# Kernel optimization log

Measured on AMD Instinct MI355X. Metric: run time of the kernel, lower is better.

The kernel has to match this reference:

```python
import jax, jax.numpy as jnp
import numpy as np

N = 2048; E = 65536; T = 6; F_IN = 2
H_ENC = 256; LAT = 128; H_DEC = 256
PRED = 6
MIN_X, MAX_X = 0.0, 1.0
MIN_Y, MAX_Y = 0.0, 1.0
MIN_EW, MAX_EW = 0.0, 0.5
VISUAL_RANGE = 0.5


def setup_inputs() -> dict:
    key = jax.random.key(0)
    ks = jax.random.split(key, 17)
    p = lambda k, shape: jax.random.normal(k, shape, jnp.float32) * 0.05
    return {
        "x_seq": jax.random.uniform(ks[0], (T, N, F_IN), jnp.float32),
        "edge_index_seq": jax.random.randint(ks[1], (T, 2, E), 0, N),
        "edge_weight_seq": jax.random.uniform(ks[2], (T, E), jnp.float32, 1e-3, 1.0),
        "h_enc": jnp.zeros((N, H_ENC), jnp.float32),
        "h_dec": jnp.zeros((N, H_DEC), jnp.float32),
        "enc_Wx": p(ks[3], (3, 2, F_IN, H_ENC)),
        "enc_bx": p(ks[4], (3, H_ENC)),
        "enc_Wh": p(ks[5], (3, 2, H_ENC, H_ENC)),
        "enc_bh": p(ks[6], (3, H_ENC)),
        "enc_lin_W": p(ks[7], (H_ENC, LAT)),
        "enc_lin_b": p(ks[8], (LAT,)),
        "dec_Wx": p(ks[9], (3, 2, LAT, H_DEC)),
        "dec_bx": p(ks[10], (3, H_DEC)),
        "dec_Wh": p(ks[11], (3, 2, H_DEC, H_DEC)),
        "dec_bh": p(ks[12], (3, H_DEC)),
        "dec_lin_W": p(ks[13], (H_DEC, F_IN)),
        "dec_lin_b": p(ks[14], (F_IN,)),
    }


def _sparse_conv_fn(edge_index, edge_weight, n):
    # ChebConv K=2, sym normalization, lambda_max=2 => T1(L_hat) = -D^-1/2 A D^-1/2
    src, dst = edge_index[0], edge_index[1]
    deg = jax.ops.segment_sum(edge_weight, src, num_segments=n)
    dinv = jnp.where(deg > 0, jax.lax.rsqrt(jnp.where(deg > 0, deg, 1.0)), 0.0)
    norm = -dinv[src] * edge_weight * dinv[dst]  # [E]

    def conv(x, W, b):  # W: [2, in, out]
        tx1 = jax.ops.segment_sum(norm[:, None] * x[src], dst, num_segments=n)
        return x @ W[0] + tx1 @ W[1] + b
    return conv


def _dense_conv_fn(y_hat):
    # graph rebuilt from detached predicted coords (radius graph, dense masked form)
    c = jax.lax.stop_gradient(y_hat)
    px = c[:, 0] * (MAX_X - MIN_X) + MIN_X
    py = c[:, 1] * (MAX_Y - MIN_Y) + MIN_Y
    coords = jnp.stack((px, py), axis=1)  # [N, 2]
    d = jnp.linalg.norm(coords[:, None, :] - coords[None, :, :], axis=2)  # [N, N]
    mask = (d < VISUAL_RANGE) & (d > 0)
    w = jnp.where(mask, (d - MIN_EW) / (MAX_EW - MIN_EW), 0.0)
    deg = w.sum(axis=1)
    dinv = jnp.where(deg > 0, jax.lax.rsqrt(jnp.where(deg > 0, deg, 1.0)), 0.0)
    M = -(dinv[:, None] * w) * dinv[None, :]  # scaled-Laplacian off-diagonal

    def conv(x, W, b):
        return x @ W[0] + (M @ x) @ W[1] + b
    return conv


def _gru(conv, x, H, Wx, bx, Wh, bh):
    # GConvGRU gates: each gate = conv_x(X) + conv_h(H)
    z = jax.nn.sigmoid(conv(x, Wx[0], bx[0]) + conv(H, Wh[0], bh[0]))
    r = jax.nn.sigmoid(conv(x, Wx[1], bx[1]) + conv(H, Wh[1], bh[1]))
    h_tilde = jnp.tanh(conv(x, Wx[2], bx[2]) + conv(H * r, Wh[2], bh[2]))
    return z * H + (1.0 - z) * h_tilde


def reference(x_seq, edge_index_seq, edge_weight_seq, h_enc, h_dec,
              enc_Wx, enc_bx, enc_Wh, enc_bh, enc_lin_W, enc_lin_b,
              dec_Wx, dec_bx, dec_Wh, dec_bh, dec_lin_W, dec_lin_b):
    n = x_seq.shape[1]

    def step(conv, x, he, hd):
        he0 = _gru(conv, x, he, enc_Wx, enc_bx, enc_Wh, enc_bh)
        z = jax.nn.relu(he0) @ enc_lin_W + enc_lin_b
        hd0 = _gru(conv, z, hd, dec_Wx, dec_bx, dec_Wh, dec_bh)
        y_hat = jax.nn.relu(hd0) @ dec_lin_W + dec_lin_b
        return y_hat, he0, hd0

    # observed snapshots (sparse edge-list graphs)
    for t in range(x_seq.shape[0]):
        conv = _sparse_conv_fn(edge_index_seq[t], edge_weight_seq[t], n)
        y_hat, h_enc, h_dec = step(conv, x_seq[t], h_enc, h_dec)

    preds = [y_hat]
    for _ in range(PRED - 1):
        conv = _dense_conv_fn(y_hat)
        y_hat, h_enc, h_dec = step(conv, y_hat, h_enc, h_dec)
        preds.append(y_hat)
    return jnp.stack(preds)  # [PRED, N, 2]
```

## Files before the change

### kernel.cpp

```cpp
#include <hip/hip_runtime.h>
#include <math.h>

#define NN 2048
#define EE 65536
#define T_OBS 6
#define FIN 2
#define HE 256
#define LT 128
#define PREDN 6
#define DMM_NZ 8
#define ZR_NZ 4
#define GT_NZ 8
#define LIN_NZ 8

typedef __attribute__((ext_vector_type(8))) short short8v;
typedef __attribute__((ext_vector_type(4))) float float4v;

static __device__ __forceinline__ unsigned short f2bf(float f) {
    union { float f; unsigned u; } v; v.f = f;
    unsigned r = v.u + 0x7fff + ((v.u >> 16) & 1);
    return (unsigned short)(r >> 16);
}

static __device__ __forceinline__ void bfsplit(float f, unsigned short& h,
                                               unsigned short& l) {
    unsigned u = __float_as_uint(f);
    h = (unsigned short)(u >> 16);
    float hf = __uint_as_float(u & 0xffff0000u);
    l = (unsigned short)(__float_as_uint(f - hf) >> 16);
}

__global__ void k_degcnt(const int* __restrict__ src, const int* __restrict__ dst,
                         const float* __restrict__ ew,
                         float* __restrict__ deg, int* __restrict__ cnt) {
    int e = blockIdx.x * blockDim.x + threadIdx.x;
    if (e < EE) {
        atomicAdd(&deg[src[e]], ew[e]);
        atomicAdd(&cnt[dst[e]], 1);
    }
}

__global__ void k_scan(const int* __restrict__ cnt, const float* __restrict__ deg,
                       int* __restrict__ roff, int* __restrict__ cur,
                       float* __restrict__ dinv) {
    __shared__ int part[256];
    int t = threadIdx.x;
#pragma unroll
    for (int i = t; i < NN; i += 256) {
        float d = deg[i];
        dinv[i] = d > 0.f ? 1.f / sqrtf(d) : 0.f;
    }
    int loc[8];
    int s = 0;
#pragma unroll
    for (int i = 0; i < 8; i++) { loc[i] = cnt[t * 8 + i]; s += loc[i]; }
    part[t] = s;
    __syncthreads();
    for (int off = 1; off < 256; off <<= 1) {
        int v = (t >= off) ? part[t - off] : 0;
        __syncthreads();
        part[t] += v;
        __syncthreads();
    }
    int run = (t == 0) ? 0 : part[t - 1];
#pragma unroll
    for (int i = 0; i < 8; i++) {
        int idx = t * 8 + i;
        roff[idx] = run;
        cur[idx] = run;
        run += loc[i];
    }
    if (t == 255) roff[NN] = run;
}

__global__ void k_scatter2(const int* __restrict__ src, const int* __restrict__ dst,
                           const float* __restrict__ ew, const float* __restrict__ dinv,
                           int* __restrict__ cur,
                           int* __restrict__ csr_src, float* __restrict__ csr_nrm) {
    int e = blockIdx.x * blockDim.x + threadIdx.x;
    if (e < EE) {
        int s = src[e], d = dst[e];
        int p = atomicAdd(&cur[d], 1);
        csr_src[p] = s;
        csr_nrm[p] = -dinv[s] * ew[e] * dinv[d];
    }
}

template <int F>
__global__ void k_spmm_v(const int* __restrict__ roff, const int* __restrict__ csr_src,
                         const float* __restrict__ csr_nrm,
                         const float* __restrict__ X, float* __restrict__ out) {
    int w = threadIdx.x >> 6, lane = threadIdx.x & 63;
    int nid = (blockIdx.x << 2) + w;
    int c = lane << 2;
    int s0 = roff[nid], s1 = roff[nid + 1];
    float4 acc = make_float4(0.f, 0.f, 0.f, 0.f);
    int s = s0;
    for (; s + 8 <= s1; s += 8) {
        int is[8]; float ws[8];
#pragma unroll
        for (int j = 0; j < 8; j++) { is[j] = csr_src[s + j]; ws[j] = csr_nrm[s + j]; }
        if (c < F) {
            float4 xv[8];
#pragma unroll
            for (int j = 0; j < 8; j++) xv[j] = *(const float4*)&X[(size_t)is[j] * F + c];
#pragma unroll
            for (int j = 0; j < 8; j++) {
                acc.x = fmaf(ws[j], xv[j].x, acc.x);
                acc.y = fmaf(ws[j], xv[j].y, acc.y);
                acc.z = fmaf(ws[j], xv[j].z, acc.z);
                acc.w = fmaf(ws[j], xv[j].w, acc.w);
            }
        }
    }
    for (; s < s1; ++s) {
        int i0 = csr_src[s]; float w0 = csr_nrm[s];
        if (c < F) {
            float4 xv = *(const float4*)&X[(size_t)i0 * F + c];
            acc.x = fmaf(w0, xv.x, acc.x);
            acc.y = fmaf(w0, xv.y, acc.y);
            acc.z = fmaf(w0, xv.z, acc.z);
            acc.w = fmaf(w0, xv.w, acc.w);
        }
    }
    if (c < F) *(float4*)&out[(size_t)nid * F + c] = acc;
}

__global__ void k_spmm2(const int* __restrict__ roff, const int* __restrict__ csr_src,
                        const float* __restrict__ csr_nrm,
                        const float* __restrict__ X, float* __restrict__ out) {
    int nid = blockIdx.x * blockDim.x + threadIdx.x;
    if (nid < NN) {
        int s0 = roff[nid], s1 = roff[nid + 1];
        float a0 = 0.f, a1 = 0.f;
        for (int s = s0; s < s1; ++s) {
            int i = csr_src[s]; float w = csr_nrm[s];
            float2 xv = *(const float2*)&X[2 * i];
            a0 = fmaf(w, xv.x, a0);
            a1 = fmaf(w, xv.y, a1);
        }
        out[2 * nid] = a0;
        out[2 * nid + 1] = a1;
    }
}

__global__ void k_ddeg(const float* __restrict__ c, float* __restrict__ dinv) {
    int i = blockIdx.x;
    int t = threadIdx.x;
    float xi = c[2 * i], yi = c[2 * i + 1];
    float s = 0.f;
    for (int j = t; j < NN; j += 256) {
        float dx = xi - c[2 * j], dy = yi - c[2 * j + 1];
        float d = sqrtf(dx * dx + dy * dy);
        if (d > 0.f && d < 0.5f) s += 2.f * d;
    }
    __shared__ float red[256];
    red[t] = s;
    __syncthreads();
    for (int off = 128; off > 0; off >>= 1) {
        if (t < off) red[t] += red[t + off];
        __syncthreads();
    }
    if (t == 0) {
        float d = red[0];
        dinv[i] = d > 0.f ? 1.f / sqrtf(d) : 0.f;
    }
}

__global__ void k_dM(const float* __restrict__ c, const float* __restrict__ dinv,
                     float* __restrict__ M, unsigned short* __restrict__ Mb) {
    int idx = blockIdx.x * blockDim.x + threadIdx.x;
    int i = idx >> 11, j = idx & (NN - 1);
    float dx = c[2 * i] - c[2 * j], dy = c[2 * i + 1] - c[2 * j + 1];
    float d = sqrtf(dx * dx + dy * dy);
    float w = (d > 0.f && d < 0.5f) ? 2.f * d : 0.f;
    float v = -(dinv[i] * w) * dinv[j];
    M[idx] = v;
    Mb[idx] = f2bf(v);
}

template <int F>
__global__ __launch_bounds__(256) void k_dmm_mf(
    const unsigned short* __restrict__ Mb, const float* __restrict__ X,
    float* __restrict__ pbuf)
{
    __shared__ __align__(16) unsigned short Ms[64][72];
    __shared__ __align__(16) unsigned short Xs[64][72];
    const int tid = threadIdx.x;
    const int wid = tid >> 6, lane = tid & 63;
    const int m0 = blockIdx.x << 6, n0 = blockIdx.y << 6;
    const int kb0 = blockIdx.z << 8;
    const int lr = lane & 15;
    const int kg = lane >> 4;
    float4v acc[4];
#pragma unroll
    for (int t = 0; t < 4; t++) acc[t] = (float4v){0.f, 0.f, 0.f, 0.f};

    for (int kb = kb0; kb < kb0 + 256; kb += 64) {
#pragma unroll
        for (int it = 0; it < 2; it++) {
            int i = tid + it * 256;
            int r = i >> 3, c8 = (i & 7) << 3;
            *(short8v*)&Ms[r][c8] =
                *(const short8v*)&Mb[(size_t)(m0 + r) * NN + kb + c8];
        }
#pragma unroll
        for (int it = 0; it < 2; it++) {
            int i = tid + it * 256;
            int k2 = (i & 31) << 1;
            int n4 = (i >> 5) << 2;
            float4 va = *(const float4*)&X[(size_t)(kb + k2) * F + n0 + n4];
            float4 vb = *(const float4*)&X[(size_t)(kb + k2 + 1) * F + n0 + n4];
            unsigned pk;
            pk = (unsigned)f2bf(va.x) | ((unsigned)f2bf(vb.x) << 16);
            *(unsigned*)&Xs[n4 + 0][k2] = pk;
            pk = (unsigned)f2bf(va.y) | ((unsigned)f2bf(vb.y) << 16);
            *(unsigned*)&Xs[n4 + 1][k2] = pk;
            pk = (unsigned)f2bf(va.z) | ((unsigned)f2bf(vb.z) << 16);
            *(unsigned*)&Xs[n4 + 2][k2] = pk;
            pk = (unsigned)f2bf(va.w) | ((unsigned)f2bf(vb.w) << 16);
            *(unsigned*)&Xs[n4 + 3][k2] = pk;
        }
        __syncthreads();
#pragma unroll
        for (int kh = 0; kh < 2; kh++) {
            int kk = kh * 32 + kg * 8;
            short8v a = *(const short8v*)&Ms[(wid << 4) + lr][kk];
#pragma unroll
            for (int t = 0; t < 4; t++) {
                short8v b = *(const short8v*)&Xs[(t << 4) + lr][kk];
                acc[t] = __builtin_amdgcn_mfma_f32_16x16x32_bf16(a, b, acc[t], 0, 0, 0);
            }
        }
        __syncthreads();
    }
    float* p = pbuf + (size_t)blockIdx.z * NN * F;
#pragma unroll
    for (int t = 0; t < 4; t++)
#pragma unroll
        for (int j = 0; j < 4; j++)
            p[(size_t)(m0 + (wid << 4) + (kg << 2) + j) * F + n0 + (t << 4) + lr] =
                acc[t][j];
}

template <int F, int NZ>
__global__ void k_redks(const float* __restrict__ pbuf, float* __restrict__ out) {
    const int TOT = NN * F / 4;
    int i = blockIdx.x * blockDim.x + threadIdx.x;
    if (i < TOT) {
        const float4* p = (const float4*)pbuf;
        float4 s = p[i];
#pragma unroll
        for (int z = 1; z < NZ; z++) {
            float4 v = p[(size_t)z * TOT + i];
            s.x += v.x; s.y += v.y; s.z += v.z; s.w += v.w;
        }
        ((float4*)out)[i] = s;
    }
}

__global__ void k_dmv2(const float* __restrict__ M, const float* __restrict__ X,
                       float* __restrict__ out) {
    int i = blockIdx.x;
    int t = threadIdx.x;
    float a0 = 0.f, a1 = 0.f;
    for (int j = t; j < NN; j += 256) {
        float m = M[i * NN + j];
        a0 = fmaf(m, X[2 * j], a0);
        a1 = fmaf(m, X[2 * j + 1], a1);
    }
    __shared__ float r0[256], r1[256];
    r0[t] = a0;
    r1[t] = a1;
    __syncthreads();
    for (int off = 128; off > 0; off >>= 1) {
        if (t < off) { r0[t] += r0[t + off]; r1[t] += r1[t + off]; }
        __syncthreads();
    }
    if (t == 0) { out[2 * i] = r0[0]; out[2 * i + 1] = r1[0]; }
}

template <bool RELU>
__device__ __forceinline__ void mfma_seg(
    unsigned short (*Ah)[40], unsigned short (*Al)[40],
    unsigned short (*Bh)[40], unsigned short (*Bl)[40],
    const float* __restrict__ A, int lda,
    const float* __restrict__ B, int ldb, int K,
    int m0, int tid, int wid, int lr, int kg, float4v (&acc)[4])
{
    for (int k0 = 0; k0 < K; k0 += 32) {
        {
            int r = tid >> 2, k8 = (tid & 3) << 3;
            const float* ap = &A[(size_t)(m0 + r) * lda + k0 + k8];
            float4 va = *(const float4*)ap;
            float4 vb = *(const float4*)(ap + 4);
            float v[8] = {va.x, va.y, va.z, va.w, vb.x, vb.y, vb.z, vb.w};
            short8v hv, lv;
#pragma unroll
            for (int j = 0; j < 8; j++) {
                float f = RELU ? fmaxf(v[j], 0.f) : v[j];
                unsigned short h, l;
                bfsplit(f, h, l);
                hv[j] = (short)h; lv[j] = (short)l;
            }
            *(short8v*)&Ah[r][k8] = hv;
            *(short8v*)&Al[r][k8] = lv;
        }
        {
            int k2 = (tid & 15) << 1;
            int n4 = (tid >> 4) << 2;
            const float* bp = &B[(size_t)(k0 + k2) * ldb + n4];
            float4 va = *(const float4*)bp;
            float4 vb = *(const float4*)(bp + ldb);
            float v0[4] = {va.x, va.y, va.z, va.w};
            float v1[4] = {vb.x, vb.y, vb.z, vb.w};
#pragma unroll
            for (int j = 0; j < 4; j++) {
                unsigned short h0, l0, h1, l1;
                bfsplit(v0[j], h0, l0);
                bfsplit(v1[j], h1, l1);
                *(unsigned*)&Bh[n4 + j][k2] = (unsigned)h0 | ((unsigned)h1 << 16);
                *(unsigned*)&Bl[n4 + j][k2] = (unsigned)l0 | ((unsigned)l1 << 16);
            }
        }
        __syncthreads();
        short8v ah = *(short8v*)&Ah[(wid << 4) + lr][kg << 3];
        short8v al = *(short8v*)&Al[(wid << 4) + lr][kg << 3];
#pragma unroll
        for (int t = 0; t < 4; t++) {
            short8v bh = *(short8v*)&Bh[(t << 4) + lr][kg << 3];
            short8v bl = *(short8v*)&Bl[(t << 4) + lr][kg << 3];
            acc[t] = __builtin_amdgcn_mfma_f32_16x16x32_bf16(ah, bh, acc[t], 0, 0, 0);
            acc[t] = __builtin_amdgcn_mfma_f32_16x16x32_bf16(ah, bl, acc[t], 0, 0, 0);
            acc[t] = __builtin_amdgcn_mfma_f32_16x16x32_bf16(al, bh, acc[t], 0, 0, 0);
        }
        __syncthreads();
    }
}

__global__ __launch_bounds__(256) void k_zr_ks(
    const float* __restrict__ A0, int K01, const float* __restrict__ A1,
    const float* __restrict__ H, const float* __restrict__ A3,
    const float* __restrict__ Wx, const float* __restrict__ Wh,
    float* __restrict__ pbuf)
{
    __shared__ __align__(16) unsigned short Ah[64][40], Al[64][40],
                                            Bh[64][40], Bl[64][40];
    int tid = threadIdx.x;
    int wid = tid >> 6, lane = tid & 63, lr = lane & 15, kg = lane >> 4;
    int m0 = blockIdx.x << 6;
    int g = blockIdx.y >> 2;
    int n0 = (blockIdx.y & 3) << 6;
    float4v acc[4];
#pragma unroll
    for (int t = 0; t < 4; t++) acc[t] = (float4v){0.f, 0.f, 0.f, 0.f};
    const float* As[4] = {A0, A1, H, A3};
    const int ldas[4] = {K01, K01, HE, HE};
    const float* Bs[4] = {
        Wx + (size_t)(g * 2 + 0) * K01 * HE + n0,
        Wx + (size_t)(g * 2 + 1) * K01 * HE + n0,
        Wh + (size_t)(g * 2 + 0) * HE * HE + n0,
        Wh + (size_t)(g * 2 + 1) * HE * HE + n0};
    const int Ks[4] = {K01, K01, HE, HE};
    int chunk = (2 * K01 + 2 * HE) / ZR_NZ;
    int lo = blockIdx.z * chunk, hi = lo + chunk;
    int off = 0;
#pragma unroll
    for (int s = 0; s < 4; s++) {
        int a = lo - off; a = a < 0 ? 0 : a;
        int b = hi - off; b = b > Ks[s] ? Ks[s] : b;
        if (b > a)
            mfma_seg<false>(Ah, Al, Bh, Bl, As[s] + a, ldas[s],
                            Bs[s] + (size_t)a * HE, HE, b - a,
                            m0, tid, wid, lr, kg, acc);
        off += Ks[s];
    }
    float* p = pbuf + (size_t)blockIdx.z * NN * 512;
    int cbase = (g << 8) + n0;
#pragma unroll
    for (int t = 0; t < 4; t++)
#pragma unroll
        for (int j = 0; j < 4; j++)
            p[(size_t)(m0 + (wid << 4) + (kg << 2) + j) * 512 + cbase + (t << 4) + lr] =
                acc[t][j];
}

__global__ void k_zr_ep(const float* __restrict__ pbuf,
                        const float* __restrict__ bx, const float* __restrict__ bh,
                        const float* __restrict__ H,
                        const float* __restrict__ x2, const float* __restrict__ ax2,
                        const float* __restrict__ Wx,
                        float* __restrict__ gz, float* __restrict__ hr)
{
    int i = blockIdx.x * 256 + threadIdx.x;
    const float4* p = (const float4*)pbuf;
    const size_t S = (size_t)NN * 512 / 4;
    float4 a = p[i];
#pragma unroll
    for (int z = 1; z < ZR_NZ; z++) {
        float4 v = p[(size_t)z * S + i];
        a.x += v.x; a.y += v.y; a.z += v.z; a.w += v.w;
    }
    int row = i >> 7, c = (i & 127) << 2;
    int g = c >> 8, cc = c & 255;
    if (Wx) {
        float x0 = x2[2 * row], x1 = x2[2 * row + 1];
        float q0 = ax2[2 * row], q1 = ax2[2 * row + 1];
        const float* W0 = Wx + (size_t)(g * 2 + 0) * FIN * HE;
        const float* W1 = Wx + (size_t)(g * 2 + 1) * FIN * HE;
        float4 w00 = *(const float4*)&W0[cc];
        float4 w01 = *(const float4*)&W0[HE + cc];
        float4 w10 = *(const float4*)&W1[cc];
        float4 w11 = *(const float4*)&W1[HE + cc];
        a.x += x0 * w00.x + x1 * w01.x + q0 * w10.x + q1 * w11.x;
        a.y += x0 * w00.y + x1 * w01.y + q0 * w10.y + q1 * w11.y;
        a.z += x0 * w00.z + x1 * w01.z + q0 * w10.z + q1 * w11.z;
        a.w += x0 * w00.w + x1 * w01.w + q0 * w10.w + q1 * w11.w;
    }
    float4 b0 = *(const float4*)&bx[c];
    float4 b1 = *(const float4*)&bh[c];
    float4 s;
    s.x = 1.f / (1.f + expf(-(a.x + b0.x + b1.x)));
    s.y = 1.f / (1.f + expf(-(a.y + b0.y + b1.y)));
    s.z = 1.f / (1.f + expf(-(a.z + b0.z + b1.z)));
    s.w = 1.f / (1.f + expf(-(a.w + b0.w + b1.w)));
    if (c < HE) {
        *(float4*)&gz[(size_t)row * HE + c] = s;
    } else {
        float4 h = *(const float4*)&H[(size_t)row * HE + cc];
        s.x *= h.x; s.y *= h.y; s.z *= h.z; s.w *= h.w;
        *(float4*)&hr[(size_t)row * HE + cc] = s;
    }
}

__global__ __launch_bounds__(256) void k_gt_ks(
    const float* __restrict__ A0, int K01, const float* __restrict__ A1,
    const float* __restrict__ hr, const float* __restrict__ A3,
    const float* __restrict__ Wx2, const float* __restrict__ Wh2,
    float* __restrict__ pbuf)
{
    __shared__ __align__(16) unsigned short Ah[64][40], Al[64][40],
                                            Bh[64][40], Bl[64][40];
    int tid = threadIdx.x;
    int wid = tid >> 6, lane = tid & 63, lr = lane & 15, kg = lane >> 4;
    int m0 = blockIdx.x << 6;
    int n0 = blockIdx.y << 6;
    float4v acc[4];
#pragma unroll
    for (int t = 0; t < 4; t++) acc[t] = (float4v){0.f, 0.f, 0.f, 0.f};
    const float* As[4] = {A0, A1, hr, A3};
    const int ldas[4] = {K01, K01, HE, HE};
    const float* Bs[4] = {
        Wx2 + n0,
        Wx2 + (size_t)K01 * HE + n0,
        Wh2 + n0,
        Wh2 + (size_t)HE * HE + n0};
    const int Ks[4] = {K01, K01, HE, HE};
    int chunk = (2 * K01 + 2 * HE) / GT_NZ;
    int lo = blockIdx.z * chunk, hi = lo + chunk;
    int off = 0;
#pragma unroll
    for (int s = 0; s < 4; s++) {
        int a = lo - off; a = a < 0 ? 0 : a;
        int b = hi - off; b = b > Ks[s] ? Ks[s] : b;
        if (b > a)
            mfma_seg<false>(Ah, Al, Bh, Bl, As[s] + a, ldas[s],
                            Bs[s] + (size_t)a * HE, HE, b - a,
                            m0, tid, wid, lr, kg, acc);
        off += Ks[s];
    }
    float* p = pbuf + (size_t)blockIdx.z * NN * HE;
#pragma unroll
    for (int t = 0; t < 4; t++)
#pragma unroll
        for (int j = 0; j < 4; j++)
            p[(size_t)(m0 + (wid << 4) + (kg << 2) + j) * HE + n0 + (t << 4) + lr] =
                acc[t][j];
}

__global__ void k_gt_ep(const float* __restrict__ pbuf,
                        const float* __restrict__ bx2, const float* __restrict__ bh2,
                        const float* __restrict__ gz,
                        const float* __restrict__ x2, const float* __restrict__ ax2,
                        const float* __restrict__ Wx2,
                        float* __restrict__ H)
{
    int i = blockIdx.x * 256 + threadIdx.x;
    const float4* p = (const float4*)pbuf;
    const size_t S = (size_t)NN * HE / 4;
    float4 a = p[i];
#pragma unroll
    for (int z = 1; z < GT_NZ; z++) {
        float4 v = p[(size_t)z * S + i];
        a.x += v.x; a.y += v.y; a.z += v.z; a.w += v.w;
    }
    int row = i >> 6, c = (i & 63) << 2;
    if (Wx2) {
        float x0 = x2[2 * row], x1 = x2[2 * row + 1];
        float q0 = ax2[2 * row], q1 = ax2[2 * row + 1];
        float4 w00 = *(const float4*)&Wx2[c];
        float4 w01 = *(const float4*)&Wx2[HE + c];
        float4 w10 = *(const float4*)&Wx2[2 * HE + c];
        float4 w11 = *(const float4*)&Wx2[3 * HE + c];
        a.x += x0 * w00.x + x1 * w01.x + q0 * w10.x + q1 * w11.x;
        a.y += x0 * w00.y + x1 * w01.y + q0 * w10.y + q1 * w11.y;
        a.z += x0 * w00.z + x1 * w01.z + q0 * w10.z + q1 * w11.z;
        a.w += x0 * w00.w + x1 * w01.w + q0 * w10.w + q1 * w11.w;
    }
    float4 b0 = *(const float4*)&bx2[c];
    float4 b1 = *(const float4*)&bh2[c];
    size_t idx = (size_t)row * HE + c;
    float4 z = *(const float4*)&gz[idx];
    float4 h = *(const float4*)&H[idx];
    float4 o;
    o.x = z.x * h.x + (1.f - z.x) * tanhf(a.x + b0.x + b1.x);
    o.y = z.y * h.y + (1.f - z.y) * tanhf(a.y + b0.y + b1.y);
    o.z = z.z * h.z + (1.f - z.z) * tanhf(a.z + b0.z + b1.z);
    o.w = z.w * h.w + (1.f - z.w) * tanhf(a.w + b0.w + b1.w);
    *(float4*)&H[idx] = o;
}

__global__ __launch_bounds__(256) void k_lin_ks(
    const float* __restrict__ A, const float* __restrict__ B,
    float* __restrict__ pbuf)
{
    __shared__ __align__(16) unsigned short Ah[64][40], Al[64][40],
                                            Bh[64][40], Bl[64][40];
    int tid = threadIdx.x;
    int wid = tid >> 6, lane = tid & 63, lr = lane & 15, kg = lane >> 4;
    int m0 = blockIdx.x << 6;
    int n0 = blockIdx.y << 6;
    int lo = blockIdx.z << 5;
    float4v acc[4];
#pragma unroll
    for (int t = 0; t < 4; t++) acc[t] = (float4v){0.f, 0.f, 0.f, 0.f};
    mfma_seg<true>(Ah, Al, Bh, Bl, A + lo, HE, B + (size_t)lo * LT + n0, LT, 32,
                   m0, tid, wid, lr, kg, acc);
    float* p = pbuf + (size_t)blockIdx.z * NN * LT;
#pragma unroll
    for (int t = 0; t < 4; t++)
#pragma unroll
        for (int j = 0; j < 4; j++)
            p[(size_t)(m0 + (wid << 4) + (kg << 2) + j) * LT + n0 + (t << 4) + lr] =
                acc[t][j];
}

__global__ void k_lin_ep(const float* __restrict__ pbuf,
                         const float* __restrict__ bias, float* __restrict__ out)
{
    int i = blockIdx.x * 256 + threadIdx.x;
    const float4* p = (const float4*)pbuf;
    const size_t S = (size_t)NN * LT / 4;
    int c = (i & 31) << 2;
    float4 bb = *(const float4*)&bias[c];
    float4 s = make_float4(bb.x, bb.y, bb.z, bb.w);
#pragma unroll
    for (int z = 0; z < LIN_NZ; z++) {
        float4 v = p[z * S + i];
        s.x += v.x; s.y += v.y; s.z += v.z; s.w += v.w;
    }
    ((float4*)out)[i] = s;
}

__global__ void k_declin(const float* __restrict__ A, const float* __restrict__ B,
                         const float* __restrict__ bias, float* __restrict__ out) {
    int w = threadIdx.x >> 6, lane = threadIdx.x & 63;
    int m = blockIdx.x * 4 + w;
    float4 a = *(const float4*)&A[(size_t)m * HE + (lane << 2)];
    float av[4] = {a.x, a.y, a.z, a.w};
    float a0 = 0.f, a1 = 0.f;
#pragma unroll
    for (int j = 0; j < 4; j++) {
        float v = fmaxf(av[j], 0.f);
        float2 b = *(const float2*)&B[((lane << 2) + j) * 2];
        a0 = fmaf(v, b.x, a0);
        a1 = fmaf(v, b.y, a1);
    }
    for (int off = 32; off > 0; off >>= 1) {
        a0 += __shfl_down(a0, off, 64);
        a1 += __shfl_down(a1, off, 64);
    }
    if (lane == 0) {
        out[2 * m] = a0 + bias[0];
        out[2 * m + 1] = a1 + bias[1];
    }
}

extern "C" void kernel_launch(void* const* d_in, const int* in_sizes, int n_in,
                              void* d_out, int out_size, void* d_ws, size_t ws_size,
                              hipStream_t stream) {
    (void)in_sizes; (void)n_in; (void)out_size; (void)ws_size;
    const float* x_seq = (const float*)d_in[0];
    const int* ei = (const int*)d_in[1];
    const float* ews = (const float*)d_in[2];
    const float* h_enc_in = (const float*)d_in[3];
    const float* h_dec_in = (const float*)d_in[4];
    const float* encWx = (const float*)d_in[5];
    const float* encbx = (const float*)d_in[6];
    const float* encWh = (const float*)d_in[7];
    const float* encbh = (const float*)d_in[8];
    const float* elinW = (const float*)d_in[9];
    const float* elinb = (const float*)d_in[10];
    const float* decWx = (const float*)d_in[11];
    const float* decbx = (const float*)d_in[12];
    const float* decWh = (const float*)d_in[13];
    const float* decbh = (const float*)d_in[14];
    const float* dlinW = (const float*)d_in[15];
    const float* dlinb = (const float*)d_in[16];
    float* out = (float*)d_out;

    float* W = (float*)d_ws;
    float* h_enc = W; W += (size_t)NN * HE;
    float* h_dec = W; W += (size_t)NN * HE;
    float* aggx  = W; W += (size_t)NN * HE;
    float* aggh  = W; W += (size_t)NN * HE;
    float* hr    = W; W += (size_t)NN * HE;
    float* agghr = W; W += (size_t)NN * HE;
    float* gz    = W; W += (size_t)NN * HE;
    float* zlat  = W; W += (size_t)NN * LT;
    float* yhat  = W; W += (size_t)NN * FIN;
    float* deg   = W; W += NN;
    int*   cnt   = (int*)W; W += NN;
    float* dinv  = W; W += NN;
    float* csr_nrm = W; W += EE;
    float* Mm    = W; W += (size_t)NN * NN;
    unsigned short* Mb = (unsigned short*)W; W += (size_t)NN * NN / 2;
    float* pbuf  = W; W += (size_t)ZR_NZ * NN * 512;
    int* roff = (int*)W;
    int* cur  = roff + (NN + 2);
    int* csr_src = cur + NN;

    hipMemcpyAsync(h_enc, h_enc_in, sizeof(float) * NN * HE, hipMemcpyDeviceToDevice, stream);
    hipMemcpyAsync(h_dec, h_dec_in, sizeof(float) * NN * HE, hipMemcpyDeviceToDevice, stream);

    for (int step = 0; step < T_OBS + PREDN - 1; ++step) {
        bool sparse = step < T_OBS;
        const float* xin;
        if (sparse) {
            const int* srcp = ei + (size_t)step * 2 * EE;
            const int* dstp = srcp + EE;
            const float* ewt = ews + (size_t)step * EE;
            hipMemsetAsync(deg, 0, sizeof(float) * NN * 2, stream);
            k_degcnt<<<EE / 256, 256, 0, stream>>>(srcp, dstp, ewt, deg, cnt);
            k_scan<<<1, 256, 0, stream>>>(cnt, deg, roff, cur, dinv);
            k_scatter2<<<EE / 256, 256, 0, stream>>>(srcp, dstp, ewt, dinv, cur,
                                                     csr_src, csr_nrm);
            xin = x_seq + (size_t)step * NN * FIN;
        } else {
            k_ddeg<<<NN, 256, 0, stream>>>(yhat, dinv);
            k_dM<<<(NN * NN) / 256, 256, 0, stream>>>(yhat, dinv, Mm, Mb);
            xin = yhat;
        }

        if (sparse) k_spmm2<<<NN / 256, 256, 0, stream>>>(roff, csr_src, csr_nrm, xin, aggx);
        else        k_dmv2<<<NN, 256, 0, stream>>>(Mm, xin, aggx);
        if (sparse) {
            k_spmm_v<HE><<<NN / 4, 256, 0, stream>>>(roff, csr_src, csr_nrm, h_enc, aggh);
        } else {
            k_dmm_mf<HE><<<dim3(NN / 64, HE / 64, DMM_NZ), 256, 0, stream>>>(Mb, h_enc, pbuf);
            k_redks<HE, DMM_NZ><<<NN * HE / 4 / 256, 256, 0, stream>>>(pbuf, aggh);
        }
        k_zr_ks<<<dim3(NN / 64, 8, ZR_NZ), 256, 0, stream>>>(xin, 0, aggx, h_enc, aggh,
                                                             encWx, encWh, pbuf);
        k_zr_ep<<<NN * 512 / 4 / 256, 256, 0, stream>>>(pbuf, encbx, encbh, h_enc,
                                                        xin, aggx, encWx, gz, hr);
        if (sparse) {
            k_spmm_v<HE><<<NN / 4, 256, 0, stream>>>(roff, csr_src, csr_nrm, hr, agghr);
        } else {
            k_dmm_mf<HE><<<dim3(NN / 64, HE / 64, DMM_NZ), 256, 0, stream>>>(Mb, hr, pbuf);
            k_redks<HE, DMM_NZ><<<NN * HE / 4 / 256, 256, 0, stream>>>(pbuf, agghr);
        }
        k_gt_ks<<<dim3(NN / 64, 4, GT_NZ), 256, 0, stream>>>(xin, 0, aggx, hr, agghr,
                                                             encWx + 4 * FIN * HE,
                                                             encWh + 4 * HE * HE, pbuf);
        k_gt_ep<<<NN * HE / 4 / 256, 256, 0, stream>>>(pbuf, encbx + 2 * HE,
                                                       encbh + 2 * HE, gz,
                                                       xin, aggx, encWx + 4 * FIN * HE,
                                                       h_enc);
        k_lin_ks<<<dim3(NN / 64, 2, LIN_NZ), 256, 0, stream>>>(h_enc, elinW, pbuf);
        k_lin_ep<<<NN * LT / 4 / 256, 256, 0, stream>>>(pbuf, elinb, zlat);

        if (sparse) {
            k_spmm_v<LT><<<NN / 4, 256, 0, stream>>>(roff, csr_src, csr_nrm, zlat, aggx);
        } else {
            k_dmm_mf<LT><<<dim3(NN / 64, LT / 64, DMM_NZ), 256, 0, stream>>>(Mb, zlat, pbuf);
            k_redks<LT, DMM_NZ><<<NN * LT / 4 / 256, 256, 0, stream>>>(pbuf, aggx);
        }
        if (sparse) {
            k_spmm_v<HE><<<NN / 4, 256, 0, stream>>>(roff, csr_src, csr_nrm, h_dec, aggh);
        } else {
            k_dmm_mf<HE><<<dim3(NN / 64, HE / 64, DMM_NZ), 256, 0, stream>>>(Mb, h_dec, pbuf);
            k_redks<HE, DMM_NZ><<<NN * HE / 4 / 256, 256, 0, stream>>>(pbuf, aggh);
        }
        k_zr_ks<<<dim3(NN / 64, 8, ZR_NZ), 256, 0, stream>>>(zlat, LT, aggx, h_dec, aggh,
                                                             decWx, decWh, pbuf);
        k_zr_ep<<<NN * 512 / 4 / 256, 256, 0, stream>>>(pbuf, decbx, decbh, h_dec,
                                                        nullptr, nullptr, nullptr, gz, hr);
        if (sparse) {
            k_spmm_v<HE><<<NN / 4, 256, 0, stream>>>(roff, csr_src, csr_nrm, hr, agghr);
        } else {
            k_dmm_mf<HE><<<dim3(NN / 64, HE / 64, DMM_NZ), 256, 0, stream>>>(Mb, hr, pbuf);
            k_redks<HE, DMM_NZ><<<NN * HE / 4 / 256, 256, 0, stream>>>(pbuf, agghr);
        }
        k_gt_ks<<<dim3(NN / 64, 4, GT_NZ), 256, 0, stream>>>(zlat, LT, aggx, hr, agghr,
                                                             decWx + 4 * LT * HE,
                                                             decWh + 4 * HE * HE, pbuf);
        k_gt_ep<<<NN * HE / 4 / 256, 256, 0, stream>>>(pbuf, decbx + 2 * HE,
                                                       decbh + 2 * HE, gz,
                                                       nullptr, nullptr, nullptr,
                                                       h_dec);
        k_declin<<<NN / 4, 256, 0, stream>>>(h_dec, dlinW, dlinb, yhat);

        if (step >= T_OBS - 1) {
            hipMemcpyAsync(out + (size_t)(step - (T_OBS - 1)) * NN * FIN, yhat,
                           sizeof(float) * NN * FIN, hipMemcpyDeviceToDevice, stream);
        }
    }
}
```

Measured before the change: 1.983 ms.

## Batch sparse graph preprocessing across all observed steps and drop fp32 dense matrix

The per-step CSR construction (degree count, scan, scatter) and the input-feature aggregation for all six observed snapshots are moved into single batched launches before the recurrent loop, using per-step buffers. This cuts roughly 25 small serial launches down to about 5 and lets the graph work run in parallel across snapshots. The dense rollout no longer writes a 16MB fp32 adjacency matrix; the 2-column matvec reads the bf16 matrix instead, which roughly halves that memory traffic but lowers the matvec's precision to bf16.

```diff
diff --git a/kernel.cpp b/kernel.cpp
--- a/kernel.cpp
+++ b/kernel.cpp
@@ -30,20 +30,33 @@
     l = (unsigned short)(__float_as_uint(f - hf) >> 16);
 }
 
-__global__ void k_degcnt(const int* __restrict__ src, const int* __restrict__ dst,
-                         const float* __restrict__ ew,
-                         float* __restrict__ deg, int* __restrict__ cnt) {
+static __device__ __forceinline__ float bf2f(unsigned short b) {
+    return __uint_as_float(((unsigned)b) << 16);
+}
+
+__global__ void k_degcnt_b(const int* __restrict__ ei, const float* __restrict__ ews,
+                           float* __restrict__ deg_all, int* __restrict__ cnt_all) {
+    int t = blockIdx.y;
     int e = blockIdx.x * blockDim.x + threadIdx.x;
+    const int* src = ei + (size_t)t * 2 * EE;
+    const int* dst = src + EE;
+    const float* ew = ews + (size_t)t * EE;
     if (e < EE) {
-        atomicAdd(&deg[src[e]], ew[e]);
-        atomicAdd(&cnt[dst[e]], 1);
-    }
-}
-
-__global__ void k_scan(const int* __restrict__ cnt, const float* __restrict__ deg,
-                       int* __restrict__ roff, int* __restrict__ cur,
-                       float* __restrict__ dinv) {
+        atomicAdd(&deg_all[t * NN + src[e]], ew[e]);
+        atomicAdd(&cnt_all[t * NN + dst[e]], 1);
+    }
+}
+
+__global__ void k_scan_b(const int* __restrict__ cnt_all, const float* __restrict__ deg_all,
+                         int* __restrict__ roff_all, int* __restrict__ cur_all,
+                         float* __restrict__ dinv_all) {
     __shared__ int part[256];
+    int tg = blockIdx.x;
+    const int* cnt = cnt_all + tg * NN;
+    const float* deg = deg_all + tg * NN;
+    int* roff = roff_all + tg * (NN + 1);
+    int* cur = cur_all + tg * NN;
+    float* dinv = dinv_all + tg * NN;
     int t = threadIdx.x;
 #pragma unroll
     for (int i = t; i < NN; i += 256) {
@@ -73,16 +86,43 @@
     if (t == 255) roff[NN] = run;
 }
 
-__global__ void k_scatter2(const int* __restrict__ src, const int* __restrict__ dst,
-                           const float* __restrict__ ew, const float* __restrict__ dinv,
-                           int* __restrict__ cur,
-                           int* __restrict__ csr_src, float* __restrict__ csr_nrm) {
+__global__ void k_scatter2_b(const int* __restrict__ ei, const float* __restrict__ ews,
+                             const float* __restrict__ dinv_all, int* __restrict__ cur_all,
+                             int* __restrict__ csr_src_all, float* __restrict__ csr_nrm_all) {
+    int tg = blockIdx.y;
     int e = blockIdx.x * blockDim.x + threadIdx.x;
+    const int* src = ei + (size_t)tg * 2 * EE;
+    const int* dst = src + EE;
+    const float* ew = ews + (size_t)tg * EE;
+    const float* dinv = dinv_all + tg * NN;
     if (e < EE) {
         int s = src[e], d = dst[e];
-        int p = atomicAdd(&cur[d], 1);
-        csr_src[p] = s;
-        csr_nrm[p] = -dinv[s] * ew[e] * dinv[d];
+        int p = atomicAdd(&cur_all[tg * NN + d], 1);
+        csr_src_all[(size_t)tg * EE + p] = s;
+        csr_nrm_all[(size_t)tg * EE + p] = -dinv[s] * ew[e] * dinv[d];
+    }
+}
+
+__global__ void k_spmm2_b(const int* __restrict__ roff_all, const int* __restrict__ csr_src_all,
+                          const float* __restrict__ csr_nrm_all, const float* __restrict__ x_seq,
+                          float* __restrict__ aggx_all) {
+    int tg = blockIdx.y;
+    int nid = blockIdx.x * blockDim.x + threadIdx.x;
+    if (nid < NN) {
+        const int* roff = roff_all + tg * (NN + 1);
+        const int* csr_src = csr_src_all + (size_t)tg * EE;
+        const float* csr_nrm = csr_nrm_all + (size_t)tg * EE;
+        const float* X = x_seq + (size_t)tg * NN * FIN;
+        int s0 = roff[nid], s1 = roff[nid + 1];
+        float a0 = 0.f, a1 = 0.f;
+        for (int s = s0; s < s1; ++s) {
+            int i = csr_src[s]; float w = csr_nrm[s];
+            float2 xv = *(const float2*)&X[2 * i];
+            a0 = fmaf(w, xv.x, a0);
+            a1 = fmaf(w, xv.y, a1);
+        }
+        aggx_all[(size_t)tg * NN * FIN + 2 * nid] = a0;
+        aggx_all[(size_t)tg * NN * FIN + 2 * nid + 1] = a1;
     }
 }
 
@@ -126,24 +166,6 @@
     if (c < F) *(float4*)&out[(size_t)nid * F + c] = acc;
 }
 
-__global__ void k_spmm2(const int* __restrict__ roff, const int* __restrict__ csr_src,
-                        const float* __restrict__ csr_nrm,
-                        const float* __restrict__ X, float* __restrict__ out) {
-    int nid = blockIdx.x * blockDim.x + threadIdx.x;
-    if (nid < NN) {
-        int s0 = roff[nid], s1 = roff[nid + 1];
-        float a0 = 0.f, a1 = 0.f;
-        for (int s = s0; s < s1; ++s) {
-            int i = csr_src[s]; float w = csr_nrm[s];
-            float2 xv = *(const float2*)&X[2 * i];
-            a0 = fmaf(w, xv.x, a0);
-            a1 = fmaf(w, xv.y, a1);
-        }
-        out[2 * nid] = a0;
-        out[2 * nid + 1] = a1;
-    }
-}
-
 __global__ void k_ddeg(const float* __restrict__ c, float* __restrict__ dinv) {
     int i = blockIdx.x;
     int t = threadIdx.x;
@@ -168,15 +190,13 @@
 }
 
 __global__ void k_dM(const float* __restrict__ c, const float* __restrict__ dinv,
-                     float* __restrict__ M, unsigned short* __restrict__ Mb) {
+                     unsigned short* __restrict__ Mb) {
     int idx = blockIdx.x * blockDim.x + threadIdx.x;
     int i = idx >> 11, j = idx & (NN - 1);
     float dx = c[2 * i] - c[2 * j], dy = c[2 * i + 1] - c[2 * j + 1];
     float d = sqrtf(dx * dx + dy * dy);
     float w = (d > 0.f && d < 0.5f) ? 2.f * d : 0.f;
-    float v = -(dinv[i] * w) * dinv[j];
-    M[idx] = v;
-    Mb[idx] = f2bf(v);
+    Mb[idx] = f2bf(-(dinv[i] * w) * dinv[j]);
 }
 
 template <int F>
@@ -259,13 +279,13 @@
     }
 }
 
-__global__ void k_dmv2(const float* __restrict__ M, const float* __restrict__ X,
-                       float* __restrict__ out) {
+__global__ void k_dmv2b(const unsigned short* __restrict__ Mb, const float* __restrict__ X,
+                        float* __restrict__ out) {
     int i = blockIdx.x;
     int t = threadIdx.x;
     float a0 = 0.f, a1 = 0.f;
     for (int j = t; j < NN; j += 256) {
-        float m = M[i * NN + j];
+        float m = bf2f(Mb[(size_t)i * NN + j]);
         a0 = fmaf(m, X[2 * j], a0);
         a1 = fmaf(m, X[2 * j + 1], a1);
     }
@@ -619,16 +639,25 @@
     float* gz    = W; W += (size_t)NN * HE;
     float* zlat  = W; W += (size_t)NN * LT;
     float* yhat  = W; W += (size_t)NN * FIN;
-    float* deg   = W; W += NN;
-    int*   cnt   = (int*)W; W += NN;
-    float* dinv  = W; W += NN;
-    float* csr_nrm = W; W += EE;
-    float* Mm    = W; W += (size_t)NN * NN;
+    float* dinv_d = W; W += NN;
     unsigned short* Mb = (unsigned short*)W; W += (size_t)NN * NN / 2;
     float* pbuf  = W; W += (size_t)ZR_NZ * NN * 512;
-    int* roff = (int*)W;
-    int* cur  = roff + (NN + 2);
-    int* csr_src = cur + NN;
+    float* deg_all = W; W += (size_t)T_OBS * NN;
+    int*   cnt_all = (int*)W; W += (size_t)T_OBS * NN;
+    float* dinv_all = W; W += (size_t)T_OBS * NN;
+    float* csr_nrm_all = W; W += (size_t)T_OBS * EE;
+    float* aggx_all = W; W += (size_t)T_OBS * NN * FIN;
+    int* roff_all = (int*)W; W += (size_t)T_OBS * (NN + 1) + 1;
+    int* cur_all = (int*)W; W += (size_t)T_OBS * NN;
+    int* csr_src_all = (int*)W; W += (size_t)T_OBS * EE;
+
+    hipMemsetAsync(deg_all, 0, sizeof(float) * T_OBS * NN * 2, stream);
+    k_degcnt_b<<<dim3(EE / 256, T_OBS), 256, 0, stream>>>(ei, ews, deg_all, cnt_all);
+    k_scan_b<<<T_OBS, 256, 0, stream>>>(cnt_all, deg_all, roff_all, cur_all, dinv_all);
+    k_scatter2_b<<<dim3(EE / 256, T_OBS), 256, 0, stream>>>(ei, ews, dinv_all, cur_all,
+                                                            csr_src_all, csr_nrm_all);
+    k_spmm2_b<<<dim3(NN / 256, T_OBS), 256, 0, stream>>>(roff_all, csr_src_all,
+                                                         csr_nrm_all, x_seq, aggx_all);
 
     hipMemcpyAsync(h_enc, h_enc_in, sizeof(float) * NN * HE, hipMemcpyDeviceToDevice, stream);
     hipMemcpyAsync(h_dec, h_dec_in, sizeof(float) * NN * HE, hipMemcpyDeviceToDevice, stream);
@@ -636,46 +665,43 @@
     for (int step = 0; step < T_OBS + PREDN - 1; ++step) {
         bool sparse = step < T_OBS;
         const float* xin;
+        const float* aggx_s;
+        const int* roff = roff_all + step * (NN + 1);
+        const int* csr_src = csr_src_all + (size_t)step * EE;
+        const float* csr_nrm = csr_nrm_all + (size_t)step * EE;
         if (sparse) {
-            const int* srcp = ei + (size_t)step * 2 * EE;
-            const int* dstp = srcp + EE;
-            const float* ewt = ews + (size_t)step * EE;
-            hipMemsetAsync(deg, 0, sizeof(float) * NN * 2, stream);
-            k_degcnt<<<EE / 256, 256, 0, stream>>>(srcp, dstp, ewt, deg, cnt);
-            k_scan<<<1, 256, 0, stream>>>(cnt, deg, roff, cur, dinv);
-            k_scatter2<<<EE / 256, 256, 0, stream>>>(srcp, dstp, ewt, dinv, cur,
-                                                     csr_src, csr_nrm);
             xin = x_seq + (size_t)step * NN * FIN;
+            aggx_s = aggx_all + (size_t)step * NN * FIN;
         } else {
-            k_ddeg<<<NN, 256, 0, stream>>>(yhat, dinv);
-            k_dM<<<(NN * NN) / 256, 256, 0, stream>>>(yhat, dinv, Mm, Mb);
+            k_ddeg<<<NN, 256, 0, stream>>>(yhat, dinv_d);
+            k_dM<<<(NN * NN) / 256, 256, 0, stream>>>(yhat, dinv_d, Mb);
             xin = yhat;
-        }
-
-        if (sparse) k_spmm2<<<NN / 256, 256, 0, stream>>>(roff, csr_src, csr_nrm, xin, aggx);
-        else        k_dmv2<<<NN, 256, 0, stream>>>(Mm, xin, aggx);
+            k_dmv2b<<<NN, 256, 0, stream>>>(Mb, yhat, aggx);
+            aggx_s = aggx;
+        }
+
         if (sparse) {
             k_spmm_v<HE><<<NN / 4, 256, 0, stream>>>(roff, csr_src, csr_nrm, h_enc, aggh);
         } else {
             k_dmm_mf<HE><<<dim3(NN / 64, HE / 64, DMM_NZ), 256, 0, stream>>>(Mb, h_enc, pbuf);
             k_redks<HE, DMM_NZ><<<NN * HE / 4 / 256, 256, 0, stream>>>(pbuf, aggh);
         }
-        k_zr_ks<<<dim3(NN / 64, 8, ZR_NZ), 256, 0, stream>>>(xin, 0, aggx, h_enc, aggh,
+        k_zr_ks<<<dim3(NN / 64, 8, ZR_NZ), 256, 0, stream>>>(xin, 0, aggx_s, h_enc, aggh,
                                                              encWx, encWh, pbuf);
         k_zr_ep<<<NN * 512 / 4 / 256, 256, 0, stream>>>(pbuf, encbx, encbh, h_enc,
-                                                        xin, aggx, encWx, gz, hr);
+                                                        xin, aggx_s, encWx, gz, hr);
         if (sparse) {
             k_spmm_v<HE><<<NN / 4, 256, 0, stream>>>(roff, csr_src, csr_nrm, hr, agghr);
         } else {
             k_dmm_mf<HE><<<dim3(NN / 64, HE / 64, DMM_NZ), 256, 0, stream>>>(Mb, hr, pbuf);
             k_redks<HE, DMM_NZ><<<NN * HE / 4 / 256, 256, 0, stream>>>(pbuf, agghr);
         }
-        k_gt_ks<<<dim3(NN / 64, 4, GT_NZ), 256, 0, stream>>>(xin, 0, aggx, hr, agghr,
+        k_gt_ks<<<dim3(NN / 64, 4, GT_NZ), 256, 0, stream>>>(xin, 0, aggx_s, hr, agghr,
                                                              encWx + 4 * FIN * HE,
                                                              encWh + 4 * HE * HE, pbuf);
         k_gt_ep<<<NN * HE / 4 / 256, 256, 0, stream>>>(pbuf, encbx + 2 * HE,
                                                        encbh + 2 * HE, gz,
-                                                       xin, aggx, encWx + 4 * FIN * HE,
+                                                       xin, aggx_s, encWx + 4 * FIN * HE,
                                                        h_enc);
         k_lin_ks<<<dim3(NN / 64, 2, LIN_NZ), 256, 0, stream>>>(h_enc, elinW, pbuf);
         k_lin_ep<<<NN * LT / 4 / 256, 256, 0, stream>>>(pbuf, elinb, zlat);
```

Measured after the change: 1.742 ms. 12.1% less time.
